# Kernel tuning notes

Measured on AMD Instinct MI355X. Metric: run time of the kernel, lower is better.

The kernel has to match this reference:

```python
import jax, jax.numpy as jnp
import numpy as np

N = 12000      # nodes
E = 384000     # edges (avg degree 32)
IN, HID, OUT = 128, 128, 40
BETA, ITERS = 0.5, 25   # Bjorck order-2 projection params (module defaults)


def setup_inputs() -> dict:
    key = jax.random.key(0)
    ks = jax.random.split(key, 6)
    x = jax.random.normal(ks[0], (N, IN), jnp.float32)
    edge_index = jax.random.randint(ks[1], (2, E), 0, N, dtype=jnp.int32)
    W1 = jax.random.normal(ks[2], (HID, IN), jnp.float32)
    W2 = jax.random.normal(ks[3], (HID, HID), jnp.float32)
    lin_w = jax.random.normal(ks[4], (OUT, HID), jnp.float32) / np.float32(np.sqrt(HID))
    lin_b = jax.random.normal(ks[5], (OUT,), jnp.float32) * 0.01
    return {"x": x, "W1": W1, "W2": W2, "lin_w": lin_w, "lin_b": lin_b,
            "edge_index": edge_index}


def _bjorck(w):
    # order-2 Bjorck orthonormalization (beta fixed at 0.5):
    # w <- 15/8 w - 5/4 w(w^T w) + 3/8 w(w^T w)^2
    for _ in range(ITERS):
        wtw = w.T @ w
        w = 1.875 * w - 1.25 * (w @ wtw) + 0.375 * (w @ (wtw @ wtw))
    return w


def _orthonormal(W):
    # scale_values: sqrt(||W||_inf * ||W||_1) upper-bounds the spectral norm
    # (computed on .data in torch -> stop_gradient here)
    scaling = jnp.sqrt(jnp.abs(W).sum(axis=1).max() * jnp.abs(W).sum(axis=0).max())
    scaling = jax.lax.stop_gradient(scaling)
    return _bjorck(W.T / scaling).T  # [out, in]


def _normalized_adj(edge_index):
    # to_dense_adj (scatter-add) then D^{-1/2} A^T D^{-1/2} exactly as
    # normalize_tensor_adj: adj.dot(D^{-1/2}).T.dot(D^{-1/2})
    r, c = edge_index[0], edge_index[1]
    adj = jnp.zeros((N, N), jnp.float32).at[r, c].add(1.0)
    rowsum = adj.sum(axis=1)
    d = jnp.where(rowsum > 0, rowsum ** -0.5, 0.0)
    return d[:, None] * adj.T * d[None, :]


def reference(x, W1, W2, lin_w, lin_b, edge_index):
    norm_adj = _normalized_adj(edge_index)          # [N, N]
    h = jax.nn.relu(norm_adj @ (x @ _orthonormal(W1).T))   # [N, HID]
    h = jax.nn.relu(norm_adj @ (h @ _orthonormal(W2).T))   # [N, HID]
    # dropout inactive (eval mode)
    logits = h @ lin_w.T + lin_b                    # [N, OUT]
    return jax.nn.log_softmax(logits, axis=1)
```

## Files before the change

kernel.cpp:

```cpp
#include <hip/hip_runtime.h>
#include <math.h>

#define NN 12000
#define EE 384000
#define FF 128
#define NOUT 40
#define BJ_MAX 25
#define NWARM 8
#define EXIT_TOL 3e-3f
#define GEMM_BLOCKS ((NN + 63) / 64)
#define SEG1 3
#define SEG2 6
#define SEG3 9
#define NDB 64
#define ESL (EE / NDB)
#define ESL4 (ESL / 4)
#define DHALF 6000

typedef __attribute__((ext_vector_type(8))) short bf16x8;
typedef __attribute__((ext_vector_type(4))) short s16x4;
typedef __attribute__((ext_vector_type(4))) float f32x4;
typedef unsigned short ushort_t;

__device__ __forceinline__ ushort_t f2bf(float x) {
  unsigned u = __float_as_uint(x);
  unsigned r = (u + 0x7FFFu + ((u >> 16) & 1u)) >> 16;
  return (ushort_t)r;
}
__device__ __forceinline__ float bf2f(ushort_t h) {
  return __uint_as_float(((unsigned)h) << 16);
}
__device__ __forceinline__ int swz(int r, int c) {
  return ((r << 8) + (c << 1)) ^ ((r & 7) << 4);
}

__device__ __forceinline__ void mm_product(const char* Xh, const char* Xl,
    const char* Yh, const char* Yl, int R0, int C0, int lane, f32x4 (&acc)[2][4]) {
  int rl = lane & 15;
  int kq = (lane >> 4) * 8;
  #pragma unroll
  for (int k0 = 0; k0 < 128; k0 += 32) {
    bf16x8 ah[2], al[2];
    #pragma unroll
    for (int i = 0; i < 2; i++) {
      ah[i] = *(const bf16x8*)(Xh + swz(R0 + i * 16 + rl, k0 + kq));
      al[i] = *(const bf16x8*)(Xl + swz(R0 + i * 16 + rl, k0 + kq));
    }
    #pragma unroll
    for (int j = 0; j < 4; j++) {
      bf16x8 bh = *(const bf16x8*)(Yh + swz(C0 + j * 16 + rl, k0 + kq));
      bf16x8 bl = *(const bf16x8*)(Yl + swz(C0 + j * 16 + rl, k0 + kq));
      #pragma unroll
      for (int i = 0; i < 2; i++) {
        acc[i][j] = __builtin_amdgcn_mfma_f32_16x16x32_bf16(ah[i], bh, acc[i][j], 0, 0, 0);
        acc[i][j] = __builtin_amdgcn_mfma_f32_16x16x32_bf16(ah[i], bl, acc[i][j], 0, 0, 0);
        acc[i][j] = __builtin_amdgcn_mfma_f32_16x16x32_bf16(al[i], bh, acc[i][j], 0, 0, 0);
      }
    }
  }
}

__device__ __forceinline__ void store_C(char* Ch, char* Cl, int R0, int C0,
    int lane, f32x4 (&acc)[2][4]) {
  int cl = lane & 15, rq = (lane >> 4) * 4;
  #pragma unroll
  for (int i = 0; i < 2; i++)
  #pragma unroll
  for (int j = 0; j < 4; j++) {
    int col = C0 + j * 16 + cl;
    int row = R0 + i * 16 + rq;
    s16x4 hv, lv;
    #pragma unroll
    for (int t = 0; t < 4; t++) {
      float x = acc[i][j][t];
      ushort_t h = f2bf(x);
      ushort_t lo = f2bf(x - bf2f(h));
      hv[t] = (short)h; lv[t] = (short)lo;
    }
    *(s16x4*)(Ch + swz(col, row)) = hv;
    *(s16x4*)(Cl + swz(col, row)) = lv;
  }
}

__device__ __forceinline__ void store_CR(char* Ch, char* Cl, char* Rh, char* Rl,
    int R0, int C0, int lane, f32x4 (&acc)[2][4], float oscale) {
  int cl = lane & 15, rq = (lane >> 4) * 4;
  #pragma unroll
  for (int i = 0; i < 2; i++)
  #pragma unroll
  for (int j = 0; j < 4; j++) {
    int col = C0 + j * 16 + cl;
    int row = R0 + i * 16 + rq;
    s16x4 hv, lv;
    #pragma unroll
    for (int t = 0; t < 4; t++) {
      float x = acc[i][j][t] * oscale;
      ushort_t h = f2bf(x);
      ushort_t lo = f2bf(x - bf2f(h));
      hv[t] = (short)h; lv[t] = (short)lo;
    }
    *(s16x4*)(Ch + swz(col, row)) = hv;
    *(s16x4*)(Cl + swz(col, row)) = lv;
    #pragma unroll
    for (int t = 0; t < 4; t++) {
      *(ushort_t*)(Rh + swz(row + t, col)) = (ushort_t)(unsigned short)hv[t];
      *(ushort_t*)(Rl + swz(row + t, col)) = (ushort_t)(unsigned short)lv[t];
    }
  }
}

__device__ void bjorck_segment(char* lds, float* wred, int L, int s_it, int e_it,
    int is_last, const float* __restrict__ W1, const float* __restrict__ W2,
    ushort_t* __restrict__ wfc, char* __restrict__ state) {
  char* P0h = lds;
  char* P0l = lds + 32768;
  char* P1h = lds + 65536;
  char* P1l = lds + 98304;
  const float* Wsrc = (L == 0) ? W1 : W2;
  int tid = threadIdx.x;
  int lane = tid & 63;
  int wv = tid >> 6;
  int R0 = (wv >> 1) * 32;
  int C0 = (wv & 1) * 64;
  char* st = state + L * 131072;
  float inv_s = 1.0f;

  if (s_it == 0) {
    int r = tid >> 2, c0 = (tid & 3) * 32;
    float rsum = 0.0f;
    #pragma unroll
    for (int mm = 0; mm < 32; mm += 8) {
      const float4* xp4 = (const float4*)(Wsrc + r * FF + c0 + mm);
      float4 v0 = xp4[0];
      float4 v1 = xp4[1];
      float xv[8] = {v0.x, v0.y, v0.z, v0.w, v1.x, v1.y, v1.z, v1.w};
      bf16x8 hv, lv;
      #pragma unroll
      for (int t = 0; t < 8; t++) {
        ushort_t h = f2bf(xv[t]);
        hv[t] = (short)h;
        lv[t] = (short)f2bf(xv[t] - bf2f(h));
        rsum += fabsf(xv[t]);
      }
      *(bf16x8*)(P0h + swz(r, c0 + mm)) = hv;
      *(bf16x8*)(P0l + swz(r, c0 + mm)) = lv;
      #pragma unroll
      for (int t = 0; t < 8; t++) {
        *(ushort_t*)(P1h + swz(c0 + mm + t, r)) = (ushort_t)(unsigned short)hv[t];
        *(ushort_t*)(P1l + swz(c0 + mm + t, r)) = (ushort_t)(unsigned short)lv[t];
      }
    }
    rsum += __shfl_xor(rsum, 1);
    rsum += __shfl_xor(rsum, 2);
    if ((tid & 3) == 0) wred[8 + r] = rsum;
    __syncthreads();
    {
      int c = tid >> 2;
      float csum = 0.0f;
      #pragma unroll
      for (int mm = 0; mm < 32; mm += 8) {
        bf16x8 hv = *(const bf16x8*)(P1h + swz(c, c0 + mm));
        #pragma unroll
        for (int t = 0; t < 8; t++) csum += fabsf(bf2f((ushort_t)(unsigned short)hv[t]));
      }
      csum += __shfl_xor(csum, 1);
      csum += __shfl_xor(csum, 2);
      if ((tid & 3) == 0) wred[136 + c] = csum;
    }
    __syncthreads();
    if (tid < 256) {
      float v = wred[8 + tid];
      #pragma unroll
      for (int off = 32; off; off >>= 1) v = fmaxf(v, __shfl_xor(v, off));
      if ((tid & 63) == 0) wred[266 + (tid >> 6)] = v;
    }
    __syncthreads();
    if (tid == 0) {
      float rm = fmaxf(wred[266], wred[267]);
      float cm = fmaxf(wred[268], wred[269]);
      wred[264] = 1.0f / sqrtf(rm * cm);
    }
    __syncthreads();
    inv_s = wred[264];
  } else {
    int4* dst = (int4*)lds;
    const int4* src = (const int4*)st;
    for (int i = tid; i < 8192; i += 512) dst[i] = src[i];
    __syncthreads();
  }

  int done = 0;
  for (int it = s_it; it < e_it; it++) {
    float ca, cb, cc, oscale = 1.0f;
    if (it < NWARM)       { ca = 3.4445f; cb = -4.7750f; cc = 2.0315f; }
    else if (it == NWARM) { ca = 2.1479f; cb = -1.7258f; cc = 0.5645f; }
    else                  { ca = 1.875f;  cb = -1.25f;   cc = 0.375f; }
    if (it == 0) {
      float is2 = inv_s * inv_s;
      cb *= is2;
      cc *= is2 * is2;
      oscale = inv_s;
    }

    f32x4 m_acc[2][4] = {};
    mm_product(P0h, P0l, P0h, P0l, R0, C0, lane, m_acc);

    if (it > NWARM) {
      int cl = lane & 15, rq = (lane >> 4) * 4;
      float lmax = 0.0f;
      #pragma unroll
      for (int i = 0; i < 2; i++)
      #pragma unroll
      for (int j = 0; j < 4; j++)
      #pragma unroll
      for (int t = 0; t < 4; t++) {
        int row = R0 + i * 16 + rq + t;
        int col = C0 + j * 16 + cl;
        float d = m_acc[i][j][t] - ((row == col) ? 1.0f : 0.0f);
        lmax = fmaxf(lmax, fabsf(d));
      }
      #pragma unroll
      for (int off = 32; off; off >>= 1) lmax = fmaxf(lmax, __shfl_xor(lmax, off));
      if (lane == 0) wred[wv] = lmax;
      __syncthreads();
      float gmax = 0.0f;
      #pragma unroll
      for (int w = 0; w < 8; w++) gmax = fmaxf(gmax, wred[w]);
      if (gmax < EXIT_TOL) { done = 1; break; }
    } else {
      __syncthreads();
    }
    store_C(P0h, P0l, R0, C0, lane, m_acc);
    __syncthreads();

    f32x4 p_acc[2][4] = {};
    mm_product(P0h, P0l, P0h, P0l, R0, C0, lane, p_acc);
    {
      int cl = lane & 15, rq = (lane >> 4) * 4;
      #pragma unroll
      for (int i = 0; i < 2; i++)
      #pragma unroll
      for (int j = 0; j < 4; j++)
      #pragma unroll
      for (int t = 0; t < 4; t++) {
        int row = R0 + i * 16 + rq + t;
        int col = C0 + j * 16 + cl;
        float pv = cb * m_acc[i][j][t] + cc * p_acc[i][j][t];
        if (row == col) pv += ca;
        p_acc[i][j][t] = pv;
      }
    }
    __syncthreads();
    store_C(P0h, P0l, R0, C0, lane, p_acc);
    __syncthreads();

    f32x4 v_acc[2][4] = {};
    mm_product(P0h, P0l, P1h, P1l, R0, C0, lane, v_acc);
    __syncthreads();
    store_CR(P1h, P1l, P0h, P0l, R0, C0, lane, v_acc, oscale);
    __syncthreads();
  }

  if (done || is_last) {
    ushort_t* oh = wfc + L * 32768;
    ushort_t* ol = oh + 16384;
    int r = tid >> 2;
    int q = tid & 3;
    #pragma unroll
    for (int b = 0; b < 4; b++) {
      int c0 = q * 32 + b * 8;
      bf16x8 hv = *(const bf16x8*)(P0h + swz(r, c0));
      bf16x8 lv = *(const bf16x8*)(P0l + swz(r, c0));
      *(bf16x8*)(oh + r * FF + c0) = hv;
      *(bf16x8*)(ol + r * FF + c0) = lv;
    }
  } else {
    const int4* src = (const int4*)lds;
    int4* dst = (int4*)st;
    for (int i = tid; i < 8192; i += 512) dst[i] = src[i];
  }
}

__global__ __launch_bounds__(512) void k1_seg_deg(const int* __restrict__ ei,
    int* __restrict__ pr, int* __restrict__ pc,
    const float* __restrict__ W1, const float* __restrict__ W2,
    ushort_t* __restrict__ wfc, char* __restrict__ state) {
  __shared__ char lds[131072];
  __shared__ float wred[272];
  if (blockIdx.x >= 2) {
    int b = blockIdx.x - 2;
    int type = b >> 6;
    int sl = b & 63;
    int* hist = (int*)lds;
    int tid = threadIdx.x;
    for (int i = tid; i < 12000; i += 512) hist[i] = 0;
    __syncthreads();
    const int4* e4 = (const int4*)(ei + (type ? 0 : EE)) + sl * ESL4;
    for (int i = tid; i < ESL4; i += 512) {
      int4 v = e4[i];
      atomicAdd(&hist[v.x], 1); atomicAdd(&hist[v.y], 1);
      atomicAdd(&hist[v.z], 1); atomicAdd(&hist[v.w], 1);
    }
    __syncthreads();
    int* dst = (type ? pr : pc) + sl * 12000;
    for (int i = tid; i < 12000; i += 512) dst[i] = hist[i];
    return;
  }
  bjorck_segment(lds, wred, blockIdx.x, 0, SEG1, 0, W1, W2, wfc, state);
}

__global__ __launch_bounds__(512) void k2_seg_scan(const int* __restrict__ pr,
    const int* __restrict__ pc, int* __restrict__ rowstart, float* __restrict__ dinv,
    int* __restrict__ pcsum,
    const float* __restrict__ W1, const float* __restrict__ W2,
    ushort_t* __restrict__ wfc, char* __restrict__ state) {
  __shared__ char lds[131072];
  __shared__ float wred[272];
  int tid = threadIdx.x;
  if (blockIdx.x == 2) {
    int* tot = (int*)lds;
    int* sums = tot + 12000;
    for (int i = tid; i < 12000; i += 512) {
      int v = 0;
      #pragma unroll
      for (int b = 0; b < NDB; b++) v += pc[b * 12000 + i];
      tot[i] = v;
    }
    __syncthreads();
    const int CH = 24;
    int base = tid * CH;
    int s = 0;
    int local[CH];
    #pragma unroll
    for (int m = 0; m < CH; m++) {
      int idx = base + m;
      int v = (idx < NN) ? tot[idx] : 0;
      local[m] = s;
      s += v;
    }
    sums[tid] = s;
    __syncthreads();
    for (int off = 1; off < 512; off <<= 1) {
      int v = (tid >= off) ? sums[tid - off] : 0;
      __syncthreads();
      sums[tid] += v;
      __syncthreads();
    }
    int excl = (tid > 0) ? sums[tid - 1] : 0;
    #pragma unroll
    for (int m = 0; m < CH; m++) {
      int idx = base + m;
      if (idx < NN) rowstart[idx] = excl + local[m];
    }
    if (tid == 511) rowstart[NN] = sums[511];
    return;
  }
  if (blockIdx.x == 3) {
    for (int i = tid; i < NN; i += 512) {
      int dv = 0;
      #pragma unroll
      for (int b = 0; b < NDB; b++) dv += pr[b * 12000 + i];
      dinv[i] = (dv > 0) ? (1.0f / sqrtf((float)dv)) : 0.0f;
    }
    return;
  }
  if (blockIdx.x >= 4) {
    int i0 = (blockIdx.x - 4) * 3000;
    for (int i = i0 + tid; i < i0 + 3000; i += 512) {
      int run = 0;
      #pragma unroll
      for (int b = 0; b < NDB; b++) {
        int v = pc[b * 12000 + i];
        pcsum[b * 12000 + i] = run;
        run += v;
      }
    }
    return;
  }
  bjorck_segment(lds, wred, blockIdx.x, SEG1, SEG2, 0, W1, W2, wfc, state);
}

__global__ __launch_bounds__(512) void k3_seg_scatter(const int* __restrict__ ei,
    const int* __restrict__ rowstart, const int* __restrict__ pcsum,
    int* __restrict__ srcl,
    const float* __restrict__ W1, const float* __restrict__ W2,
    ushort_t* __restrict__ wfc, char* __restrict__ state) {
  __shared__ char lds[131072];
  __shared__ float wred[272];
  if (blockIdx.x >= 2) {
    int b = blockIdx.x - 2;
    int sl = b >> 1;
    int dbase = (b & 1) * DHALF;
    int* co = (int*)lds;
    int* fillL = co + DHALF;
    int tid = threadIdx.x;
    const int* ps = pcsum + sl * 12000 + dbase;
    const int* rs = rowstart + dbase;
    for (int i = tid; i < DHALF; i += 512) {
      co[i] = rs[i] + ps[i];
      fillL[i] = 0;
    }
    __syncthreads();
    const int4* r4 = (const int4*)ei + sl * ESL4;
    const int4* c4 = (const int4*)(ei + EE) + sl * ESL4;
    for (int i = tid; i < ESL4; i += 512) {
      int4 cv = c4[i];
      int4 rv = r4[i];
      int d;
      d = cv.x - dbase;
      if ((unsigned)d < (unsigned)DHALF) srcl[co[d] + atomicAdd(&fillL[d], 1)] = rv.x;
      d = cv.y - dbase;
      if ((unsigned)d < (unsigned)DHALF) srcl[co[d] + atomicAdd(&fillL[d], 1)] = rv.y;
      d = cv.z - dbase;
      if ((unsigned)d < (unsigned)DHALF) srcl[co[d] + atomicAdd(&fillL[d], 1)] = rv.z;
      d = cv.w - dbase;
      if ((unsigned)d < (unsigned)DHALF) srcl[co[d] + atomicAdd(&fillL[d], 1)] = rv.w;
    }
    return;
  }
  bjorck_segment(lds, wred, blockIdx.x, SEG2, SEG3, 0, W1, W2, wfc, state);
}

__global__ __launch_bounds__(512) void k4_seg_spmm(const float* __restrict__ X,
    float* __restrict__ Sout, const float* __restrict__ dinv,
    const int* __restrict__ rowstart, const int* __restrict__ srcl,
    const float* __restrict__ W1, const float* __restrict__ W2,
    ushort_t* __restrict__ wfc, char* __restrict__ state) {
  __shared__ char lds[131072];
  __shared__ float wred[272];
  if (blockIdx.x >= 2) {
    int g = threadIdx.x >> 5, lane32 = threadIdx.x & 31;
    int row = (blockIdx.x - 2) * 16 + g;
    int s = rowstart[row], e = rowstart[row + 1];
    const float4* G4 = (const float4*)X;
    float4 a0 = make_float4(0.f, 0.f, 0.f, 0.f);
    float4 a1 = make_float4(0.f, 0.f, 0.f, 0.f);
    int p = s;
    for (; p + 2 <= e; p += 2) {
      int r0 = srcl[p], r1 = srcl[p + 1];
      float d0 = dinv[r0], d1 = dinv[r1];
      float4 g0 = G4[r0 * 32 + lane32];
      float4 g1 = G4[r1 * 32 + lane32];
      a0.x += d0 * g0.x; a0.y += d0 * g0.y; a0.z += d0 * g0.z; a0.w += d0 * g0.w;
      a1.x += d1 * g1.x; a1.y += d1 * g1.y; a1.z += d1 * g1.z; a1.w += d1 * g1.w;
    }
    if (p < e) {
      int r0 = srcl[p];
      float d0 = dinv[r0];
      float4 g0 = G4[r0 * 32 + lane32];
      a0.x += d0 * g0.x; a0.y += d0 * g0.y; a0.z += d0 * g0.z; a0.w += d0 * g0.w;
    }
    float dc = dinv[row];
    float4 o;
    o.x = dc * (a0.x + a1.x); o.y = dc * (a0.y + a1.y);
    o.z = dc * (a0.z + a1.z); o.w = dc * (a0.w + a1.w);
    ((float4*)Sout)[row * 32 + lane32] = o;
    return;
  }
  bjorck_segment(lds, wred, blockIdx.x, SEG3, BJ_MAX, 1, W1, W2, wfc, state);
}

__global__ __launch_bounds__(256) void gemm_fused(const float* __restrict__ S,
    const ushort_t* __restrict__ wc1, const ushort_t* __restrict__ wc2,
    float* __restrict__ Out) {
  __shared__ char xlds[65536];
  char* Sh = xlds;
  char* Sl = xlds + 16384;
  char* Hh = xlds + 32768;
  char* Hl = xlds + 49152;
  int tid = threadIdx.x;
  int row0 = blockIdx.x * 64;

  {
    int r = tid >> 2;
    int q = (tid & 3) * 32;
    int gr = row0 + r;
    #pragma unroll
    for (int b = 0; b < 32; b += 8) {
      bf16x8 hv, lv;
      if (gr < NN) {
        const float4* xp4 = (const float4*)(S + gr * FF + q + b);
        float4 v0 = xp4[0];
        float4 v1 = xp4[1];
        float xv[8] = {v0.x, v0.y, v0.z, v0.w, v1.x, v1.y, v1.z, v1.w};
        #pragma unroll
        for (int t = 0; t < 8; t++) {
          ushort_t h = f2bf(xv[t]);
          hv[t] = (short)h;
          lv[t] = (short)f2bf(xv[t] - bf2f(h));
        }
      } else {
        #pragma unroll
        for (int t = 0; t < 8; t++) { hv[t] = 0; lv[t] = 0; }
      }
      *(bf16x8*)(Sh + swz(r, q + b)) = hv;
      *(bf16x8*)(Sl + swz(r, q + b)) = lv;
    }
  }
  __syncthreads();

  int lane = tid & 63, wv = tid >> 6;
  int R0 = (wv & 1) * 32;
  int C0 = (wv >> 1) * 64;
  int rl = lane & 15, kq = (lane >> 4) * 8;

  {
    f32x4 acc[2][4] = {};
    #pragma unroll
    for (int k0 = 0; k0 < 128; k0 += 32) {
      bf16x8 ah[2], al[2];
      #pragma unroll
      for (int i = 0; i < 2; i++) {
        ah[i] = *(const bf16x8*)(Sh + swz(R0 + i * 16 + rl, k0 + kq));
        al[i] = *(const bf16x8*)(Sl + swz(R0 + i * 16 + rl, k0 + kq));
      }
      #pragma unroll
      for (int j = 0; j < 4; j++) {
        const ushort_t* bp = wc1 + (C0 + j * 16 + rl) * FF + k0 + kq;
        bf16x8 bh = *(const bf16x8*)bp;
        bf16x8 bl = *(const bf16x8*)(bp + 16384);
        #pragma unroll
        for (int i = 0; i < 2; i++) {
          acc[i][j] = __builtin_amdgcn_mfma_f32_16x16x32_bf16(ah[i], bh, acc[i][j], 0, 0, 0);
          acc[i][j] = __builtin_amdgcn_mfma_f32_16x16x32_bf16(ah[i], bl, acc[i][j], 0, 0, 0);
          acc[i][j] = __builtin_amdgcn_mfma_f32_16x16x32_bf16(al[i], bh, acc[i][j], 0, 0, 0);
        }
      }
    }
    int rq = (lane >> 4) * 4;
    #pragma unroll
    for (int i = 0; i < 2; i++)
    #pragma unroll
    for (int j = 0; j < 4; j++) {
      int c = C0 + j * 16 + rl;
      #pragma unroll
      for (int t = 0; t < 4; t++) {
        int r = R0 + i * 16 + rq + t;
        float x = fmaxf(acc[i][j][t], 0.0f);
        ushort_t h = f2bf(x);
        ushort_t lo = f2bf(x - bf2f(h));
        *(ushort_t*)(Hh + swz(r, c)) = h;
        *(ushort_t*)(Hl + swz(r, c)) = lo;
      }
    }
  }
  __syncthreads();

  {
    f32x4 acc[2][4] = {};
    #pragma unroll
    for (int k0 = 0; k0 < 128; k0 += 32) {
      bf16x8 ah[2], al[2];
      #pragma unroll
      for (int i = 0; i < 2; i++) {
        ah[i] = *(const bf16x8*)(Hh + swz(R0 + i * 16 + rl, k0 + kq));
        al[i] = *(const bf16x8*)(Hl + swz(R0 + i * 16 + rl, k0 + kq));
      }
      #pragma unroll
      for (int j = 0; j < 4; j++) {
        const ushort_t* bp = wc2 + (C0 + j * 16 + rl) * FF + k0 + kq;
        bf16x8 bh = *(const bf16x8*)bp;
        bf16x8 bl = *(const bf16x8*)(bp + 16384);
        #pragma unroll
        for (int i = 0; i < 2; i++) {
          acc[i][j] = __builtin_amdgcn_mfma_f32_16x16x32_bf16(ah[i], bh, acc[i][j], 0, 0, 0);
          acc[i][j] = __builtin_amdgcn_mfma_f32_16x16x32_bf16(ah[i], bl, acc[i][j], 0, 0, 0);
          acc[i][j] = __builtin_amdgcn_mfma_f32_16x16x32_bf16(al[i], bh, acc[i][j], 0, 0, 0);
        }
      }
    }
    int rq = (lane >> 4) * 4;
    #pragma unroll
    for (int i = 0; i < 2; i++)
    #pragma unroll
    for (int j = 0; j < 4; j++) {
      int col = C0 + j * 16 + rl;
      #pragma unroll
      for (int t = 0; t < 4; t++) {
        int node = row0 + R0 + i * 16 + rq + t;
        if (node < NN) Out[node * FF + col] = acc[i][j][t];
      }
    }
  }
}

__global__ __launch_bounds__(256) void spmm_head(const float* __restrict__ G,
    const float* __restrict__ dinv, const int* __restrict__ rowstart,
    const int* __restrict__ srcl, const float* __restrict__ lw,
    const float* __restrict__ lb, float* __restrict__ out) {
  __shared__ float slw[NOUT * 130];
  __shared__ float slb[64];
  __shared__ float sh[8][128];
  int tid = threadIdx.x;
  for (int i = tid; i < NOUT * 32; i += 256) {
    int r = i >> 5, c4 = i & 31;
    float4 v = ((const float4*)lw)[r * 32 + c4];
    float* dst = slw + r * 130 + c4 * 4;
    dst[0] = v.x; dst[1] = v.y; dst[2] = v.z; dst[3] = v.w;
  }
  if (tid < 64) slb[tid] = (tid < NOUT) ? lb[tid] : 0.0f;

  {
    int g = tid >> 5, lane32 = tid & 31;
    int row = blockIdx.x * 8 + g;
    int s = rowstart[row], e = rowstart[row + 1];
    const float4* G4 = (const float4*)G;
    float4 a0 = make_float4(0.f, 0.f, 0.f, 0.f);
    float4 a1 = make_float4(0.f, 0.f, 0.f, 0.f);
    int p = s;
    for (; p + 2 <= e; p += 2) {
      int r0 = srcl[p], r1 = srcl[p + 1];
      float d0 = dinv[r0], d1 = dinv[r1];
      float4 g0 = G4[r0 * 32 + lane32];
      float4 g1 = G4[r1 * 32 + lane32];
      a0.x += d0 * g0.x; a0.y += d0 * g0.y; a0.z += d0 * g0.z; a0.w += d0 * g0.w;
      a1.x += d1 * g1.x; a1.y += d1 * g1.y; a1.z += d1 * g1.z; a1.w += d1 * g1.w;
    }
    if (p < e) {
      int r0 = srcl[p];
      float d0 = dinv[r0];
      float4 g0 = G4[r0 * 32 + lane32];
      a0.x += d0 * g0.x; a0.y += d0 * g0.y; a0.z += d0 * g0.z; a0.w += d0 * g0.w;
    }
    float dc = dinv[row];
    float4 o;
    o.x = fmaxf(dc * (a0.x + a1.x), 0.f); o.y = fmaxf(dc * (a0.y + a1.y), 0.f);
    o.z = fmaxf(dc * (a0.z + a1.z), 0.f); o.w = fmaxf(dc * (a0.w + a1.w), 0.f);
    ((float4*)&sh[g][0])[lane32] = o;
  }
  __syncthreads();

  int lane = tid & 63, w = tid >> 6;
  int ll = (lane < NOUT) ? lane : 0;
  const float2* wrow = (const float2*)(slw + ll * 130);
  #pragma unroll
  for (int rr = 0; rr < 2; rr++) {
    int lrow = w * 2 + rr;
    int node = blockIdx.x * 8 + lrow;
    const float2* hrow = (const float2*)&sh[lrow][0];
    float val = slb[lane];
    #pragma unroll 4
    for (int k = 0; k < 64; k++) {
      float2 w2 = wrow[k];
      float2 h2 = hrow[k];
      val += w2.x * h2.x + w2.y * h2.y;
    }
    float m = (lane < NOUT) ? val : -INFINITY;
    for (int off = 32; off; off >>= 1) m = fmaxf(m, __shfl_down(m, off));
    m = __shfl(m, 0);
    float ex = (lane < NOUT) ? expf(val - m) : 0.0f;
    float ssum = ex;
    for (int off = 32; off; off >>= 1) ssum += __shfl_down(ssum, off);
    ssum = __shfl(ssum, 0);
    if (lane < NOUT) out[node * NOUT + lane] = val - m - logf(ssum);
  }
}

extern "C" void kernel_launch(void* const* d_in, const int* in_sizes, int n_in,
                              void* d_out, int out_size, void* d_ws, size_t ws_size,
                              hipStream_t stream) {
  const float* x  = (const float*)d_in[0];
  const float* W1 = (const float*)d_in[1];
  const float* W2 = (const float*)d_in[2];
  const float* lw = (const float*)d_in[3];
  const float* lb = (const float*)d_in[4];
  const int*   ei = (const int*)d_in[5];
  float* out = (float*)d_out;

  float* base = (float*)d_ws;
  float* wf   = base;
  float* dinv = wf + 32768;
  int* rowstart = (int*)(dinv + NN);
  int* srcl     = rowstart + 12004;
  float* bufA = (float*)(srcl + EE);
  float* bufB = bufA + NN * FF;
  char* state = (char*)(bufB + NN * FF);
  int* pr    = (int*)bufB;
  int* pc    = pr + NDB * 12000;
  int* pcsum = (int*)bufA;
  ushort_t* wfc = (ushort_t*)wf;

  k1_seg_deg<<<2 + 2 * NDB, 512, 0, stream>>>(ei, pr, pc, W1, W2, wfc, state);
  k2_seg_scan<<<8, 512, 0, stream>>>(pr, pc, rowstart, dinv, pcsum, W1, W2, wfc, state);
  k3_seg_scatter<<<2 + 2 * NDB, 512, 0, stream>>>(ei, rowstart, pcsum, srcl, W1, W2, wfc, state);
  k4_seg_spmm<<<2 + NN / 16, 512, 0, stream>>>(x, bufA, dinv, rowstart, srcl, W1, W2, wfc, state);

  gemm_fused<<<GEMM_BLOCKS, 256, 0, stream>>>(bufA, wfc, wfc + 32768, bufB);
  spmm_head<<<NN / 8, 256, 0, stream>>>(bufB, dinv, rowstart, srcl, lw, lb, out);
}
```

Before: 279.7 us.

## Run full Bjorck iteration in first kernel and slim later graph kernels

Moves all Bjorck orthonormalization iterations into the degree-histogram kernel instead of splitting them into segments across four kernels with global state save/restore. The scan, scatter and SpMM kernels no longer carry Bjorck blocks or the large 128KB LDS allocation, so they can run at higher occupancy. The cost is that the whole Bjorck chain now overlaps only with the histogram work rather than being hidden across the preprocessing pipeline.

```diff
diff --git a/kernel.cpp b/kernel.cpp
--- a/kernel.cpp
+++ b/kernel.cpp
@@ -9,9 +9,6 @@
 #define NWARM 8
 #define EXIT_TOL 3e-3f
 #define GEMM_BLOCKS ((NN + 63) / 64)
-#define SEG1 3
-#define SEG2 6
-#define SEG3 9
 #define NDB 64
 #define ESL (EE / NDB)
 #define ESL4 (ESL / 4)
@@ -109,9 +106,9 @@
   }
 }
 
-__device__ void bjorck_segment(char* lds, float* wred, int L, int s_it, int e_it,
-    int is_last, const float* __restrict__ W1, const float* __restrict__ W2,
-    ushort_t* __restrict__ wfc, char* __restrict__ state) {
+__device__ void bjorck_full(char* lds, float* wred, int L,
+    const float* __restrict__ W1, const float* __restrict__ W2,
+    ushort_t* __restrict__ wfc) {
   char* P0h = lds;
   char* P0l = lds + 32768;
   char* P1h = lds + 65536;
@@ -122,10 +119,8 @@
   int wv = tid >> 6;
   int R0 = (wv >> 1) * 32;
   int C0 = (wv & 1) * 64;
-  char* st = state + L * 131072;
-  float inv_s = 1.0f;
-
-  if (s_it == 0) {
+
+  {
     int r = tid >> 2, c0 = (tid & 3) * 32;
     float rsum = 0.0f;
     #pragma unroll
@@ -153,44 +148,38 @@
     rsum += __shfl_xor(rsum, 1);
     rsum += __shfl_xor(rsum, 2);
     if ((tid & 3) == 0) wred[8 + r] = rsum;
-    __syncthreads();
-    {
-      int c = tid >> 2;
-      float csum = 0.0f;
-      #pragma unroll
-      for (int mm = 0; mm < 32; mm += 8) {
-        bf16x8 hv = *(const bf16x8*)(P1h + swz(c, c0 + mm));
-        #pragma unroll
-        for (int t = 0; t < 8; t++) csum += fabsf(bf2f((ushort_t)(unsigned short)hv[t]));
-      }
-      csum += __shfl_xor(csum, 1);
-      csum += __shfl_xor(csum, 2);
-      if ((tid & 3) == 0) wred[136 + c] = csum;
-    }
-    __syncthreads();
-    if (tid < 256) {
-      float v = wred[8 + tid];
-      #pragma unroll
-      for (int off = 32; off; off >>= 1) v = fmaxf(v, __shfl_xor(v, off));
-      if ((tid & 63) == 0) wred[266 + (tid >> 6)] = v;
-    }
-    __syncthreads();
-    if (tid == 0) {
-      float rm = fmaxf(wred[266], wred[267]);
-      float cm = fmaxf(wred[268], wred[269]);
-      wred[264] = 1.0f / sqrtf(rm * cm);
-    }
-    __syncthreads();
-    inv_s = wred[264];
-  } else {
-    int4* dst = (int4*)lds;
-    const int4* src = (const int4*)st;
-    for (int i = tid; i < 8192; i += 512) dst[i] = src[i];
-    __syncthreads();
-  }
-
-  int done = 0;
-  for (int it = s_it; it < e_it; it++) {
+  }
+  __syncthreads();
+  {
+    int c = tid >> 2, c0 = (tid & 3) * 32;
+    float csum = 0.0f;
+    #pragma unroll
+    for (int mm = 0; mm < 32; mm += 8) {
+      bf16x8 hv = *(const bf16x8*)(P1h + swz(c, c0 + mm));
+      #pragma unroll
+      for (int t = 0; t < 8; t++) csum += fabsf(bf2f((ushort_t)(unsigned short)hv[t]));
+    }
+    csum += __shfl_xor(csum, 1);
+    csum += __shfl_xor(csum, 2);
+    if ((tid & 3) == 0) wred[136 + c] = csum;
+  }
+  __syncthreads();
+  if (tid < 256) {
+    float v = wred[8 + tid];
+    #pragma unroll
+    for (int off = 32; off; off >>= 1) v = fmaxf(v, __shfl_xor(v, off));
+    if ((tid & 63) == 0) wred[266 + (tid >> 6)] = v;
+  }
+  __syncthreads();
+  if (tid == 0) {
+    float rm = fmaxf(wred[266], wred[267]);
+    float cm = fmaxf(wred[268], wred[269]);
+    wred[264] = 1.0f / sqrtf(rm * cm);
+  }
+  __syncthreads();
+  float inv_s = wred[264];
+
+  for (int it = 0; it < BJ_MAX; it++) {
     float ca, cb, cc, oscale = 1.0f;
     if (it < NWARM)       { ca = 3.4445f; cb = -4.7750f; cc = 2.0315f; }
     else if (it == NWARM) { ca = 2.1479f; cb = -1.7258f; cc = 0.5645f; }
@@ -226,7 +215,7 @@
       float gmax = 0.0f;
       #pragma unroll
       for (int w = 0; w < 8; w++) gmax = fmaxf(gmax, wred[w]);
-      if (gmax < EXIT_TOL) { done = 1; break; }
+      if (gmax < EXIT_TOL) break;
     } else {
       __syncthreads();
     }
@@ -261,7 +250,7 @@
     __syncthreads();
   }
 
-  if (done || is_last) {
+  {
     ushort_t* oh = wfc + L * 32768;
     ushort_t* ol = oh + 16384;
     int r = tid >> 2;
@@ -274,17 +263,13 @@
       *(bf16x8*)(oh + r * FF + c0) = hv;
       *(bf16x8*)(ol + r * FF + c0) = lv;
     }
-  } else {
-    const int4* src = (const int4*)lds;
-    int4* dst = (int4*)st;
-    for (int i = tid; i < 8192; i += 512) dst[i] = src[i];
-  }
-}
-
-__global__ __launch_bounds__(512) void k1_seg_deg(const int* __restrict__ ei,
+  }
+}
+
+__global__ __launch_bounds__(512) void bjorck_deg(const int* __restrict__ ei,
     int* __restrict__ pr, int* __restrict__ pc,
     const float* __restrict__ W1, const float* __restrict__ W2,
-    ushort_t* __restrict__ wfc, char* __restrict__ state) {
+    ushort_t* __restrict__ wfc) {
   __shared__ char lds[131072];
   __shared__ float wred[272];
   if (blockIdx.x >= 2) {
@@ -306,19 +291,16 @@
     for (int i = tid; i < 12000; i += 512) dst[i] = hist[i];
     return;
   }
-  bjorck_segment(lds, wred, blockIdx.x, 0, SEG1, 0, W1, W2, wfc, state);
-}
-
-__global__ __launch_bounds__(512) void k2_seg_scan(const int* __restrict__ pr,
+  bjorck_full(lds, wred, blockIdx.x, W1, W2, wfc);
+}
+
+__global__ __launch_bounds__(512) void scan_all(const int* __restrict__ pr,
     const int* __restrict__ pc, int* __restrict__ rowstart, float* __restrict__ dinv,
-    int* __restrict__ pcsum,
-    const float* __restrict__ W1, const float* __restrict__ W2,
-    ushort_t* __restrict__ wfc, char* __restrict__ state) {
-  __shared__ char lds[131072];
-  __shared__ float wred[272];
+    int* __restrict__ pcsum) {
+  __shared__ int slds[12512];
   int tid = threadIdx.x;
-  if (blockIdx.x == 2) {
-    int* tot = (int*)lds;
+  if (blockIdx.x == 0) {
+    int* tot = slds;
     int* sums = tot + 12000;
     for (int i = tid; i < 12000; i += 512) {
       int v = 0;
@@ -355,7 +337,7 @@
     if (tid == 511) rowstart[NN] = sums[511];
     return;
   }
-  if (blockIdx.x == 3) {
+  if (blockIdx.x == 1) {
     for (int i = tid; i < NN; i += 512) {
       int dv = 0;
       #pragma unroll
@@ -364,100 +346,81 @@
     }
     return;
   }
-  if (blockIdx.x >= 4) {
-    int i0 = (blockIdx.x - 4) * 3000;
-    for (int i = i0 + tid; i < i0 + 3000; i += 512) {
-      int run = 0;
-      #pragma unroll
-      for (int b = 0; b < NDB; b++) {
-        int v = pc[b * 12000 + i];
-        pcsum[b * 12000 + i] = run;
-        run += v;
-      }
-    }
-    return;
-  }
-  bjorck_segment(lds, wred, blockIdx.x, SEG1, SEG2, 0, W1, W2, wfc, state);
-}
-
-__global__ __launch_bounds__(512) void k3_seg_scatter(const int* __restrict__ ei,
+  int i0 = (blockIdx.x - 2) * 3000;
+  for (int i = i0 + tid; i < i0 + 3000; i += 512) {
+    int run = 0;
+    #pragma unroll
+    for (int b = 0; b < NDB; b++) {
+      int v = pc[b * 12000 + i];
+      pcsum[b * 12000 + i] = run;
+      run += v;
+    }
+  }
+}
+
+__global__ __launch_bounds__(512) void scatter_cs(const int* __restrict__ ei,
     const int* __restrict__ rowstart, const int* __restrict__ pcsum,
-    int* __restrict__ srcl,
-    const float* __restrict__ W1, const float* __restrict__ W2,
-    ushort_t* __restrict__ wfc, char* __restrict__ state) {
-  __shared__ char lds[131072];
-  __shared__ float wred[272];
-  if (blockIdx.x >= 2) {
-    int b = blockIdx.x - 2;
-    int sl = b >> 1;
-    int dbase = (b & 1) * DHALF;
-    int* co = (int*)lds;
-    int* fillL = co + DHALF;
-    int tid = threadIdx.x;
-    const int* ps = pcsum + sl * 12000 + dbase;
-    const int* rs = rowstart + dbase;
-    for (int i = tid; i < DHALF; i += 512) {
-      co[i] = rs[i] + ps[i];
-      fillL[i] = 0;
-    }
-    __syncthreads();
-    const int4* r4 = (const int4*)ei + sl * ESL4;
-    const int4* c4 = (const int4*)(ei + EE) + sl * ESL4;
-    for (int i = tid; i < ESL4; i += 512) {
-      int4 cv = c4[i];
-      int4 rv = r4[i];
-      int d;
-      d = cv.x - dbase;
-      if ((unsigned)d < (unsigned)DHALF) srcl[co[d] + atomicAdd(&fillL[d], 1)] = rv.x;
-      d = cv.y - dbase;
-      if ((unsigned)d < (unsigned)DHALF) srcl[co[d] + atomicAdd(&fillL[d], 1)] = rv.y;
-      d = cv.z - dbase;
-      if ((unsigned)d < (unsigned)DHALF) srcl[co[d] + atomicAdd(&fillL[d], 1)] = rv.z;
-      d = cv.w - dbase;
-      if ((unsigned)d < (unsigned)DHALF) srcl[co[d] + atomicAdd(&fillL[d], 1)] = rv.w;
-    }
-    return;
-  }
-  bjorck_segment(lds, wred, blockIdx.x, SEG2, SEG3, 0, W1, W2, wfc, state);
-}
-
-__global__ __launch_bounds__(512) void k4_seg_spmm(const float* __restrict__ X,
+    int* __restrict__ srcl) {
+  __shared__ int slds[2 * DHALF];
+  int b = blockIdx.x;
+  int sl = b >> 1;
+  int dbase = (b & 1) * DHALF;
+  int* co = slds;
+  int* fillL = co + DHALF;
+  int tid = threadIdx.x;
+  const int* ps = pcsum + sl * 12000 + dbase;
+  const int* rs = rowstart + dbase;
+  for (int i = tid; i < DHALF; i += 512) {
+    co[i] = rs[i] + ps[i];
+    fillL[i] = 0;
+  }
+  __syncthreads();
+  const int4* r4 = (const int4*)ei + sl * ESL4;
+  const int4* c4 = (const int4*)(ei + EE) + sl * ESL4;
+  for (int i = tid; i < ESL4; i += 512) {
+    int4 cv = c4[i];
+    int4 rv = r4[i];
+    int d;
+    d = cv.x - dbase;
+    if ((unsigned)d < (unsigned)DHALF) srcl[co[d] + atomicAdd(&fillL[d], 1)] = rv.x;
+    d = cv.y - dbase;
+    if ((unsigned)d < (unsigned)DHALF) srcl[co[d] + atomicAdd(&fillL[d], 1)] = rv.y;
+    d = cv.z - dbase;
+    if ((unsigned)d < (unsigned)DHALF) srcl[co[d] + atomicAdd(&fillL[d], 1)] = rv.z;
+    d = cv.w - dbase;
+    if ((unsigned)d < (unsigned)DHALF) srcl[co[d] + atomicAdd(&fillL[d], 1)] = rv.w;
+  }
+}
+
+__global__ __launch_bounds__(512) void spmm_S(const float* __restrict__ X,
     float* __restrict__ Sout, const float* __restrict__ dinv,
-    const int* __restrict__ rowstart, const int* __restrict__ srcl,
-    const float* __restrict__ W1, const float* __restrict__ W2,
-    ushort_t* __restrict__ wfc, char* __restrict__ state) {
-  __shared__ char lds[131072];
-  __shared__ float wred[272];
-  if (blockIdx.x >= 2) {
-    int g = threadIdx.x >> 5, lane32 = threadIdx.x & 31;
-    int row = (blockIdx.x - 2) * 16 + g;
-    int s = rowstart[row], e = rowstart[row + 1];
-    const float4* G4 = (const float4*)X;
-    float4 a0 = make_float4(0.f, 0.f, 0.f, 0.f);
-    float4 a1 = make_float4(0.f, 0.f, 0.f, 0.f);
-    int p = s;
-    for (; p + 2 <= e; p += 2) {
-      int r0 = srcl[p], r1 = srcl[p + 1];
-      float d0 = dinv[r0], d1 = dinv[r1];
-      float4 g0 = G4[r0 * 32 + lane32];
-      float4 g1 = G4[r1 * 32 + lane32];
-      a0.x += d0 * g0.x; a0.y += d0 * g0.y; a0.z += d0 * g0.z; a0.w += d0 * g0.w;
-      a1.x += d1 * g1.x; a1.y += d1 * g1.y; a1.z += d1 * g1.z; a1.w += d1 * g1.w;
-    }
-    if (p < e) {
-      int r0 = srcl[p];
-      float d0 = dinv[r0];
-      float4 g0 = G4[r0 * 32 + lane32];
-      a0.x += d0 * g0.x; a0.y += d0 * g0.y; a0.z += d0 * g0.z; a0.w += d0 * g0.w;
-    }
-    float dc = dinv[row];
-    float4 o;
-    o.x = dc * (a0.x + a1.x); o.y = dc * (a0.y + a1.y);
-    o.z = dc * (a0.z + a1.z); o.w = dc * (a0.w + a1.w);
-    ((float4*)Sout)[row * 32 + lane32] = o;
-    return;
-  }
-  bjorck_segment(lds, wred, blockIdx.x, SEG3, BJ_MAX, 1, W1, W2, wfc, state);
+    const int* __restrict__ rowstart, const int* __restrict__ srcl) {
+  int g = threadIdx.x >> 5, lane32 = threadIdx.x & 31;
+  int row = blockIdx.x * 16 + g;
+  int s = rowstart[row], e = rowstart[row + 1];
+  const float4* G4 = (const float4*)X;
+  float4 a0 = make_float4(0.f, 0.f, 0.f, 0.f);
+  float4 a1 = make_float4(0.f, 0.f, 0.f, 0.f);
+  int p = s;
+  for (; p + 2 <= e; p += 2) {
+    int r0 = srcl[p], r1 = srcl[p + 1];
+    float d0 = dinv[r0], d1 = dinv[r1];
+    float4 g0 = G4[r0 * 32 + lane32];
+    float4 g1 = G4[r1 * 32 + lane32];
+    a0.x += d0 * g0.x; a0.y += d0 * g0.y; a0.z += d0 * g0.z; a0.w += d0 * g0.w;
+    a1.x += d1 * g1.x; a1.y += d1 * g1.y; a1.z += d1 * g1.z; a1.w += d1 * g1.w;
+  }
+  if (p < e) {
+    int r0 = srcl[p];
+    float d0 = dinv[r0];
+    float4 g0 = G4[r0 * 32 + lane32];
+    a0.x += d0 * g0.x; a0.y += d0 * g0.y; a0.z += d0 * g0.z; a0.w += d0 * g0.w;
+  }
+  float dc = dinv[row];
+  float4 o;
+  o.x = dc * (a0.x + a1.x); o.y = dc * (a0.y + a1.y);
+  o.z = dc * (a0.z + a1.z); o.w = dc * (a0.w + a1.w);
+  ((float4*)Sout)[row * 32 + lane32] = o;
 }
 
 __global__ __launch_bounds__(256) void gemm_fused(const float* __restrict__ S,
@@ -674,17 +637,15 @@
   int* srcl     = rowstart + 12004;
   float* bufA = (float*)(srcl + EE);
   float* bufB = bufA + NN * FF;
-  char* state = (char*)(bufB + NN * FF);
   int* pr    = (int*)bufB;
   int* pc    = pr + NDB * 12000;
   int* pcsum = (int*)bufA;
   ushort_t* wfc = (ushort_t*)wf;
 
-  k1_seg_deg<<<2 + 2 * NDB, 512, 0, stream>>>(ei, pr, pc, W1, W2, wfc, state);
-  k2_seg_scan<<<8, 512, 0, stream>>>(pr, pc, rowstart, dinv, pcsum, W1, W2, wfc, state);
-  k3_seg_scatter<<<2 + 2 * NDB, 512, 0, stream>>>(ei, rowstart, pcsum, srcl, W1, W2, wfc, state);
-  k4_seg_spmm<<<2 + NN / 16, 512, 0, stream>>>(x, bufA, dinv, rowstart, srcl, W1, W2, wfc, state);
-
+  bjorck_deg<<<2 + 2 * NDB, 512, 0, stream>>>(ei, pr, pc, W1, W2, wfc);
+  scan_all<<<6, 512, 0, stream>>>(pr, pc, rowstart, dinv, pcsum);
+  scatter_cs<<<2 * NDB, 512, 0, stream>>>(ei, rowstart, pcsum, srcl);
+  spmm_S<<<NN / 16, 512, 0, stream>>>(x, bufA, dinv, rowstart, srcl);
   gemm_fused<<<GEMM_BLOCKS, 256, 0, stream>>>(bufA, wfc, wfc + 32768, bufB);
   spmm_head<<<NN / 8, 256, 0, stream>>>(bufB, dinv, rowstart, srcl, lw, lb, out);
 }
```

After: 407.5 us. 45.7% more time.
